# Optimization experiments

Hardware: AMD Instinct MI355X
Metric: run time of the kernel (lower is better)

The kernel has to match this reference:

```python
import jax, jax.numpy as jnp
import numpy as np

N_NODES = 100000
N_EDGES = 1600000
D_IN = 256
D_OUT = 128


def setup_inputs() -> dict:
    key = jax.random.key(0)
    k1, k2, k3, k4, k5, k6 = jax.random.split(key, 6)
    inp = {
        "input": jax.random.normal(k1, (N_NODES, D_IN), dtype=jnp.float32),
        "edge_row": jax.random.randint(k2, (N_EDGES,), 0, N_NODES),
        "edge_col": jax.random.randint(k3, (N_EDGES,), 0, N_NODES),
        "edge_val": jax.random.uniform(k4, (N_EDGES,), dtype=jnp.float32),
        "W": jax.random.normal(k5, (D_IN, D_OUT), dtype=jnp.float32) * (1.0 / np.sqrt(D_IN)),
        "b": jax.random.normal(k6, (D_OUT,), dtype=jnp.float32) * 0.01,
    }
    return inp


def reference(input, edge_row, edge_col, edge_val, W, b):
    # support = Linear(input)  -> [N, D_OUT]
    support = jnp.dot(input, W) + b
    # sparse.mm(adj, support): out[r] = sum_e val[e] * support[col[e]] for edges with row[e]==r
    msgs = edge_val[:, None] * support[edge_col]  # [E, D_OUT]
    agg = jax.ops.segment_sum(msgs, edge_row, num_segments=N_NODES)  # [N, D_OUT]
    return jnp.tanh(agg)
```

## Files before the change

### kernel.cpp

```cpp
#include <hip/hip_runtime.h>
#include <math.h>

#define N_NODES 100000
#define N_EDGES 1600000
#define D_IN 256
#define D_OUT 128

#define OFF_SUPPORT 0
#define OFF_COUNTS  51200000
#define OFF_CSREV   51600008
#define OFF_BSUMS   64400008
#define OFF_WTHI    64400416
#define OFF_WTLO    64465952

#define SCAN_CHUNK  1024
#define SCAN_BLOCKS ((N_NODES + SCAN_CHUNK - 1) / SCAN_CHUNK)

#define GB 128
#define GEMM_BLOCKS ((N_NODES + GB - 1) / GB)
#define EDGE_BLOCKS ((N_EDGES + 255) / 256)
#define WCONV_BLOCKS ((D_IN * D_OUT) / 256)

typedef __attribute__((ext_vector_type(8))) short s8v;
typedef __attribute__((ext_vector_type(4))) float f4v;

__device__ __forceinline__ short f2bf(float x) {
  unsigned u = __float_as_uint(x);
  unsigned r = u + 0x7FFF + ((u >> 16) & 1);
  return (short)(r >> 16);
}
__device__ __forceinline__ float bf2f(short h) {
  return __uint_as_float(((unsigned)(unsigned short)h) << 16);
}

__device__ __forceinline__ void cvt8(float4 a, float4 b, s8v& h, s8v& l) {
  float f[8] = {a.x, a.y, a.z, a.w, b.x, b.y, b.z, b.w};
#pragma unroll
  for (int i = 0; i < 8; i++) {
    short hh = f2bf(f[i]);
    h[i] = hh;
    l[i] = f2bf(f[i] - bf2f(hh));
  }
}

__device__ __forceinline__ void gload_lds16(const void* g, void* l) {
  __builtin_amdgcn_global_load_lds(
      (const __attribute__((address_space(1))) void*)g,
      (__attribute__((address_space(3))) void*)l, 16, 0, 0);
}

#define VMW(N)                                             \
  asm volatile("s_waitcnt vmcnt(" #N ")" ::: "memory");    \
  __builtin_amdgcn_sched_barrier(0)
#define SBAR()                    \
  __builtin_amdgcn_s_barrier();   \
  __builtin_amdgcn_sched_barrier(0)

__global__ __launch_bounds__(256) void prep_kernel(
    const float* __restrict__ W, short* __restrict__ wt_hi,
    short* __restrict__ wt_lo, const int* __restrict__ erow,
    int* __restrict__ counts) {
  if (blockIdx.x < WCONV_BLOCKS) {
    int idx = blockIdx.x * 256 + threadIdx.x;
    int k = idx >> 7;
    int n = idx & 127;
    float v = W[idx];
    short h = f2bf(v);
    wt_hi[n * 256 + k] = h;
    wt_lo[n * 256 + k] = f2bf(v - bf2f(h));
  } else {
    int e = (blockIdx.x - WCONV_BLOCKS) * 256 + threadIdx.x;
    if (e < N_EDGES) atomicAdd(&counts[erow[e]], 1);
  }
}

__global__ __launch_bounds__(256, 2) void gemm_kernel(
    const float* __restrict__ input, const short* __restrict__ wt_hi,
    const short* __restrict__ wt_lo, const float* __restrict__ b,
    float* __restrict__ support) {
  __shared__ short Bh[2][128][64];
  __shared__ short Bl[2][128][64];
  const int t = threadIdx.x;
  const int lane = t & 63;
  const int wv = t >> 6;
  const int qm = lane & 15;
  const int quad = lane >> 4;
  const int node0 = blockIdx.x * GB;

  int r0 = node0 + wv * 32 + qm;
  int r1 = r0 + 16;
  if (r0 > N_NODES - 1) r0 = N_NODES - 1;
  if (r1 > N_NODES - 1) r1 = N_NODES - 1;
  const float* a0p = input + (size_t)r0 * D_IN + quad * 8;
  const float* a1p = input + (size_t)r1 * D_IN + quad * 8;

  const int lrow = lane >> 3;
  const int lpc = lane & 7;
  auto stageB = [&](int q, int p) {
    const int rb = wv * 32;
#pragma unroll
    for (int j = 0; j < 4; ++j) {
      int n = rb + j * 8 + lrow;
      int sc = lpc ^ (n & 7);
      const short* sh = wt_hi + (size_t)n * 256 + q * 64 + sc * 8;
      const short* sl = wt_lo + (size_t)n * 256 + q * 64 + sc * 8;
      gload_lds16(sh, &Bh[p][rb + j * 8][0]);
      gload_lds16(sl, &Bl[p][rb + j * 8][0]);
    }
  };

  float4 A0[4], A1[4], A2[4];
  auto loadA = [&](float4* d, int s) {
    d[0] = *(const float4*)(a0p + s * 32);
    d[1] = *(const float4*)(a0p + s * 32 + 4);
    d[2] = *(const float4*)(a1p + s * 32);
    d[3] = *(const float4*)(a1p + s * 32 + 4);
  };

  f4v acc[2][8];
#pragma unroll
  for (int mt = 0; mt < 2; mt++)
#pragma unroll
    for (int nt = 0; nt < 8; nt++) acc[mt][nt] = (f4v){0.f, 0.f, 0.f, 0.f};

  s8v ah0, al0, ah1, al1;
  auto cvtA = [&](const float4* X) {
    cvt8(X[0], X[1], ah0, al0);
    cvt8(X[2], X[3], ah1, al1);
  };
  auto mfma8 = [&](int p, int si) {
#pragma unroll
    for (int nt = 0; nt < 8; ++nt) {
      int n = nt * 16 + qm;
      int pc = (si * 4 + quad) ^ (n & 7);
      s8v bh = *(const s8v*)&Bh[p][n][pc * 8];
      s8v bl = *(const s8v*)&Bl[p][n][pc * 8];
      acc[0][nt] = __builtin_amdgcn_mfma_f32_16x16x32_bf16(ah0, bh, acc[0][nt], 0, 0, 0);
      acc[0][nt] = __builtin_amdgcn_mfma_f32_16x16x32_bf16(ah0, bl, acc[0][nt], 0, 0, 0);
      acc[0][nt] = __builtin_amdgcn_mfma_f32_16x16x32_bf16(al0, bh, acc[0][nt], 0, 0, 0);
      acc[1][nt] = __builtin_amdgcn_mfma_f32_16x16x32_bf16(ah1, bh, acc[1][nt], 0, 0, 0);
      acc[1][nt] = __builtin_amdgcn_mfma_f32_16x16x32_bf16(ah1, bl, acc[1][nt], 0, 0, 0);
      acc[1][nt] = __builtin_amdgcn_mfma_f32_16x16x32_bf16(al1, bh, acc[1][nt], 0, 0, 0);
    }
  };

  stageB(0, 0);
  loadA(A0, 0);
  loadA(A1, 1);
  loadA(A2, 2);
  VMW(8);
  SBAR();
  cvtA(A0);
  stageB(1, 1);
  loadA(A0, 3);
  mfma8(0, 0);
  VMW(16);
  cvtA(A1);
  loadA(A1, 4);
  mfma8(0, 1);
  VMW(8);
  SBAR();
  cvtA(A2);
  stageB(2, 0);
  loadA(A2, 5);
  mfma8(1, 0);
  VMW(16);
  cvtA(A0);
  loadA(A0, 6);
  mfma8(1, 1);
  VMW(8);
  SBAR();
  cvtA(A1);
  stageB(3, 1);
  loadA(A1, 7);
  mfma8(0, 0);
  VMW(16);
  cvtA(A2);
  mfma8(0, 1);
  VMW(4);
  SBAR();
  cvtA(A0);
  mfma8(1, 0);
  VMW(0);
  cvtA(A1);
  mfma8(1, 1);

  float bias[8];
#pragma unroll
  for (int nt = 0; nt < 8; nt++) bias[nt] = b[nt * 16 + qm];
#pragma unroll
  for (int mt = 0; mt < 2; mt++) {
#pragma unroll
    for (int nt = 0; nt < 8; nt++) {
      int col = nt * 16 + qm;
#pragma unroll
      for (int r = 0; r < 4; r++) {
        int node = node0 + wv * 32 + mt * 16 + quad * 4 + r;
        if (node < N_NODES)
          support[(size_t)node * D_OUT + col] = acc[mt][nt][r] + bias[nt];
      }
    }
  }
}

__global__ __launch_bounds__(256) void build_kernel(
    const int* __restrict__ erow, const int* __restrict__ ecol,
    const float* __restrict__ eval, const int* __restrict__ offsets,
    int* __restrict__ fill, int2* __restrict__ csr_ev) {
  int e = blockIdx.x * 256 + threadIdx.x;
  if (e < N_EDGES) {
    int r = erow[e];
    int idx = offsets[r] + atomicAdd(&fill[r], 1);
    csr_ev[idx] = make_int2(ecol[e], __float_as_int(eval[e]));
  }
}

__global__ __launch_bounds__(256) void scan_phase1(const int* __restrict__ counts,
                                                   int* __restrict__ bsums) {
  __shared__ int ts[256];
  int t = threadIdx.x;
  int idx0 = blockIdx.x * SCAN_CHUNK + t * 4;
  int s = 0;
#pragma unroll
  for (int i = 0; i < 4; i++)
    if (idx0 + i < N_NODES) s += counts[idx0 + i];
  ts[t] = s;
  __syncthreads();
#pragma unroll
  for (int off = 128; off > 0; off >>= 1) {
    if (t < off) ts[t] += ts[t + off];
    __syncthreads();
  }
  if (t == 0) bsums[blockIdx.x] = ts[0];
}

__global__ __launch_bounds__(128) void scan_phase2(int* __restrict__ bsums) {
  __shared__ int s[128];
  int t = threadIdx.x;
  int v = (t < SCAN_BLOCKS) ? bsums[t] : 0;
  s[t] = v;
  __syncthreads();
#pragma unroll
  for (int off = 1; off < 128; off <<= 1) {
    int x = (t >= off) ? s[t - off] : 0;
    __syncthreads();
    s[t] += x;
    __syncthreads();
  }
  if (t < SCAN_BLOCKS) bsums[t] = s[t] - v;
}

__global__ __launch_bounds__(256) void scan_phase3(int* __restrict__ counts,
                                                   const int* __restrict__ bsums,
                                                   int* __restrict__ fill) {
  __shared__ int ts[256];
  int t = threadIdx.x;
  int b = blockIdx.x;
  int idx0 = b * SCAN_CHUNK + t * 4;
  int v[4];
  int s = 0;
#pragma unroll
  for (int i = 0; i < 4; i++) {
    v[i] = (idx0 + i < N_NODES) ? counts[idx0 + i] : 0;
    s += v[i];
  }
  ts[t] = s;
  __syncthreads();
#pragma unroll
  for (int off = 1; off < 256; off <<= 1) {
    int x = (t >= off) ? ts[t - off] : 0;
    __syncthreads();
    ts[t] += x;
    __syncthreads();
  }
  int run = bsums[b] + ts[t] - s;
#pragma unroll
  for (int i = 0; i < 4; i++) {
    int idx = idx0 + i;
    if (idx < N_NODES) {
      counts[idx] = run;
      fill[idx] = 0;
    }
    run += v[i];
  }
  if (b == 0 && t == 0) counts[N_NODES] = N_EDGES;
}

__global__ __launch_bounds__(256) void agg_kernel(
    const int* __restrict__ offsets, const int2* __restrict__ csr_ev,
    const float* __restrict__ support, float* __restrict__ out) {
  int r = blockIdx.x * 8 + (threadIdx.x >> 5);
  int l4 = (threadIdx.x & 31) * 4;
  int beg = offsets[r];
  int end = offsets[r + 1];
  float4 acc = make_float4(0.f, 0.f, 0.f, 0.f);

  if (end > beg) {
    int2 e[8], en[8];
#pragma unroll
    for (int u = 0; u < 8; u++) {
      int idx = beg + u;
      int c = idx < end ? idx : end - 1;
      e[u] = csr_ev[c];
      if (idx >= end) e[u].y = 0;
    }
    for (int j = beg; j < end; j += 8) {
      int jn = j + 8;
      if (jn < end) {
#pragma unroll
        for (int u = 0; u < 8; u++) {
          int idx = jn + u;
          int c = idx < end ? idx : end - 1;
          en[u] = csr_ev[c];
          if (idx >= end) en[u].y = 0;
        }
      }
      float4 s[8];
#pragma unroll
      for (int u = 0; u < 8; u++)
        s[u] = *(const float4*)(support + (size_t)e[u].x * D_OUT + l4);
#pragma unroll
      for (int u = 0; u < 8; u++) {
        float v = __int_as_float(e[u].y);
        acc.x = fmaf(v, s[u].x, acc.x);
        acc.y = fmaf(v, s[u].y, acc.y);
        acc.z = fmaf(v, s[u].z, acc.z);
        acc.w = fmaf(v, s[u].w, acc.w);
      }
#pragma unroll
      for (int u = 0; u < 8; u++) e[u] = en[u];
    }
  }
  *(float4*)(out + (size_t)r * D_OUT + l4) =
      make_float4(tanhf(acc.x), tanhf(acc.y), tanhf(acc.z), tanhf(acc.w));
}

extern "C" void kernel_launch(void* const* d_in, const int* in_sizes, int n_in,
                              void* d_out, int out_size, void* d_ws, size_t ws_size,
                              hipStream_t stream) {
  const float* input = (const float*)d_in[0];
  const int* erow = (const int*)d_in[1];
  const int* ecol = (const int*)d_in[2];
  const float* eval = (const float*)d_in[3];
  const float* W = (const float*)d_in[4];
  const float* b = (const float*)d_in[5];
  float* out = (float*)d_out;

  char* ws = (char*)d_ws;
  float* support = (float*)(ws + OFF_SUPPORT);
  int* counts = (int*)(ws + OFF_COUNTS);
  int2* csr_ev = (int2*)(ws + OFF_CSREV);
  int* bsums = (int*)(ws + OFF_BSUMS);
  short* wt_hi = (short*)(ws + OFF_WTHI);
  short* wt_lo = (short*)(ws + OFF_WTLO);
  int* fill = (int*)d_out;

  hipMemsetAsync(ws + OFF_COUNTS, 0, (size_t)(N_NODES + 1) * 4, stream);

  hipLaunchKernelGGL(prep_kernel, dim3(WCONV_BLOCKS + EDGE_BLOCKS), dim3(256),
                     0, stream, W, wt_hi, wt_lo, erow, counts);
  hipLaunchKernelGGL(gemm_kernel, dim3(GEMM_BLOCKS), dim3(256), 0, stream,
                     input, wt_hi, wt_lo, b, support);
  hipLaunchKernelGGL(scan_phase1, dim3(SCAN_BLOCKS), dim3(256), 0, stream,
                     counts, bsums);
  hipLaunchKernelGGL(scan_phase2, dim3(1), dim3(128), 0, stream, bsums);
  hipLaunchKernelGGL(scan_phase3, dim3(SCAN_BLOCKS), dim3(256), 0, stream,
                     counts, bsums, fill);
  hipLaunchKernelGGL(build_kernel, dim3(EDGE_BLOCKS), dim3(256), 0, stream,
                     erow, ecol, eval, counts, fill, csr_ev);
  hipLaunchKernelGGL(agg_kernel, dim3(N_NODES / 8), dim3(256), 0, stream,
                     counts, csr_ev, support, out);
}
```

Baseline: 464.5 us.

## Fuse edge histogram into GEMM launch and reuse atomic positions in CSR build

The separate memset is removed; the counts array is now zeroed inside the weight-conversion kernel. The row-count histogram moves from the prep launch into the GEMM launch as extra blocks, so the atomics run alongside the matrix multiply. Each edge's atomicAdd return value is saved in a per-edge position array held in the output buffer, which removes the second round of atomics in the build kernel and the fill reset in the scan. Build and agg also switch to nontemporal loads and stores on packed 64-bit edge records. The cost is an extra 6.4MB position array write and read, and GEMM blocks share their launch with atomic-heavy blocks.

```diff
diff --git a/kernel.cpp b/kernel.cpp
--- a/kernel.cpp
+++ b/kernel.cpp
@@ -19,7 +19,6 @@
 #define GB 128
 #define GEMM_BLOCKS ((N_NODES + GB - 1) / GB)
 #define EDGE_BLOCKS ((N_EDGES + 255) / 256)
-#define WCONV_BLOCKS ((D_IN * D_OUT) / 256)
 
 typedef __attribute__((ext_vector_type(8))) short s8v;
 typedef __attribute__((ext_vector_type(4))) float f4v;
@@ -56,26 +55,21 @@
   __builtin_amdgcn_s_barrier();   \
   __builtin_amdgcn_sched_barrier(0)
 
-__global__ __launch_bounds__(256) void prep_kernel(
+__global__ __launch_bounds__(256) void wconv_kernel(
     const float* __restrict__ W, short* __restrict__ wt_hi,
-    short* __restrict__ wt_lo, const int* __restrict__ erow,
-    int* __restrict__ counts) {
-  if (blockIdx.x < WCONV_BLOCKS) {
-    int idx = blockIdx.x * 256 + threadIdx.x;
-    int k = idx >> 7;
-    int n = idx & 127;
-    float v = W[idx];
-    short h = f2bf(v);
-    wt_hi[n * 256 + k] = h;
-    wt_lo[n * 256 + k] = f2bf(v - bf2f(h));
-  } else {
-    int e = (blockIdx.x - WCONV_BLOCKS) * 256 + threadIdx.x;
-    if (e < N_EDGES) atomicAdd(&counts[erow[e]], 1);
-  }
-}
-
-__global__ __launch_bounds__(256, 2) void gemm_kernel(
-    const float* __restrict__ input, const short* __restrict__ wt_hi,
+    short* __restrict__ wt_lo, int* __restrict__ counts) {
+  int idx = blockIdx.x * 256 + threadIdx.x;
+  int k = idx >> 7;
+  int n = idx & 127;
+  float v = W[idx];
+  short h = f2bf(v);
+  wt_hi[n * 256 + k] = h;
+  wt_lo[n * 256 + k] = f2bf(v - bf2f(h));
+  for (int i = idx; i < N_NODES + 1; i += 32768) counts[i] = 0;
+}
+
+__device__ __forceinline__ void gemm_body(
+    int gb, const float* __restrict__ input, const short* __restrict__ wt_hi,
     const short* __restrict__ wt_lo, const float* __restrict__ b,
     float* __restrict__ support) {
   __shared__ short Bh[2][128][64];
@@ -85,7 +79,7 @@
   const int wv = t >> 6;
   const int qm = lane & 15;
   const int quad = lane >> 4;
-  const int node0 = blockIdx.x * GB;
+  const int node0 = gb * GB;
 
   int r0 = node0 + wv * 32 + qm;
   int r1 = r0 + 16;
@@ -203,15 +197,32 @@
   }
 }
 
+__global__ __launch_bounds__(256, 2) void gemm_hist_kernel(
+    const float* __restrict__ input, const short* __restrict__ wt_hi,
+    const short* __restrict__ wt_lo, const float* __restrict__ b,
+    float* __restrict__ support, const int* __restrict__ erow,
+    int* __restrict__ counts, int* __restrict__ pos_e) {
+  if (blockIdx.x < GEMM_BLOCKS) {
+    gemm_body(blockIdx.x, input, wt_hi, wt_lo, b, support);
+  } else {
+    int e = (blockIdx.x - GEMM_BLOCKS) * 256 + threadIdx.x;
+    if (e < N_EDGES) pos_e[e] = atomicAdd(&counts[erow[e]], 1);
+  }
+}
+
 __global__ __launch_bounds__(256) void build_kernel(
     const int* __restrict__ erow, const int* __restrict__ ecol,
     const float* __restrict__ eval, const int* __restrict__ offsets,
-    int* __restrict__ fill, int2* __restrict__ csr_ev) {
+    const int* __restrict__ pos_e, long long* __restrict__ csr_ev) {
   int e = blockIdx.x * 256 + threadIdx.x;
   if (e < N_EDGES) {
-    int r = erow[e];
-    int idx = offsets[r] + atomicAdd(&fill[r], 1);
-    csr_ev[idx] = make_int2(ecol[e], __float_as_int(eval[e]));
+    int r = __builtin_nontemporal_load(erow + e);
+    int c = __builtin_nontemporal_load(ecol + e);
+    int vb = __builtin_nontemporal_load((const int*)eval + e);
+    int p = __builtin_nontemporal_load(pos_e + e);
+    int idx = offsets[r] + p;
+    long long packed = (unsigned int)c | ((long long)(unsigned int)vb << 32);
+    __builtin_nontemporal_store(packed, csr_ev + idx);
   }
 }
 
@@ -251,8 +262,7 @@
 }
 
 __global__ __launch_bounds__(256) void scan_phase3(int* __restrict__ counts,
-                                                   const int* __restrict__ bsums,
-                                                   int* __restrict__ fill) {
+                                                   const int* __restrict__ bsums) {
   __shared__ int ts[256];
   int t = threadIdx.x;
   int b = blockIdx.x;
@@ -277,17 +287,14 @@
 #pragma unroll
   for (int i = 0; i < 4; i++) {
     int idx = idx0 + i;
-    if (idx < N_NODES) {
-      counts[idx] = run;
-      fill[idx] = 0;
-    }
+    if (idx < N_NODES) counts[idx] = run;
     run += v[i];
   }
   if (b == 0 && t == 0) counts[N_NODES] = N_EDGES;
 }
 
 __global__ __launch_bounds__(256) void agg_kernel(
-    const int* __restrict__ offsets, const int2* __restrict__ csr_ev,
+    const int* __restrict__ offsets, const long long* __restrict__ csr_ev,
     const float* __restrict__ support, float* __restrict__ out) {
   int r = blockIdx.x * 8 + (threadIdx.x >> 5);
   int l4 = (threadIdx.x & 31) * 4;
@@ -296,13 +303,15 @@
   float4 acc = make_float4(0.f, 0.f, 0.f, 0.f);
 
   if (end > beg) {
-    int2 e[8], en[8];
+    int ec[8], encol[8];
+    float ev[8], env[8];
 #pragma unroll
     for (int u = 0; u < 8; u++) {
       int idx = beg + u;
       int c = idx < end ? idx : end - 1;
-      e[u] = csr_ev[c];
-      if (idx >= end) e[u].y = 0;
+      long long p = __builtin_nontemporal_load(csr_ev + c);
+      ec[u] = (int)(unsigned int)p;
+      ev[u] = (idx < end) ? __uint_as_float((unsigned int)(p >> 32)) : 0.f;
     }
     for (int j = beg; j < end; j += 8) {
       int jn = j + 8;
@@ -311,24 +320,24 @@
         for (int u = 0; u < 8; u++) {
           int idx = jn + u;
           int c = idx < end ? idx : end - 1;
-          en[u] = csr_ev[c];
-          if (idx >= end) en[u].y = 0;
+          long long p = __builtin_nontemporal_load(csr_ev + c);
+          encol[u] = (int)(unsigned int)p;
+          env[u] = (idx < end) ? __uint_as_float((unsigned int)(p >> 32)) : 0.f;
         }
       }
       float4 s[8];
 #pragma unroll
       for (int u = 0; u < 8; u++)
-        s[u] = *(const float4*)(support + (size_t)e[u].x * D_OUT + l4);
+        s[u] = *(const float4*)(support + (size_t)ec[u] * D_OUT + l4);
 #pragma unroll
       for (int u = 0; u < 8; u++) {
-        float v = __int_as_float(e[u].y);
-        acc.x = fmaf(v, s[u].x, acc.x);
-        acc.y = fmaf(v, s[u].y, acc.y);
-        acc.z = fmaf(v, s[u].z, acc.z);
-        acc.w = fmaf(v, s[u].w, acc.w);
+        acc.x = fmaf(ev[u], s[u].x, acc.x);
+        acc.y = fmaf(ev[u], s[u].y, acc.y);
+        acc.z = fmaf(ev[u], s[u].z, acc.z);
+        acc.w = fmaf(ev[u], s[u].w, acc.w);
       }
 #pragma unroll
-      for (int u = 0; u < 8; u++) e[u] = en[u];
+      for (int u = 0; u < 8; u++) { ec[u] = encol[u]; ev[u] = env[u]; }
     }
   }
   *(float4*)(out + (size_t)r * D_OUT + l4) =
@@ -349,25 +358,24 @@
   char* ws = (char*)d_ws;
   float* support = (float*)(ws + OFF_SUPPORT);
   int* counts = (int*)(ws + OFF_COUNTS);
-  int2* csr_ev = (int2*)(ws + OFF_CSREV);
+  long long* csr_ev = (long long*)(ws + OFF_CSREV);
   int* bsums = (int*)(ws + OFF_BSUMS);
   short* wt_hi = (short*)(ws + OFF_WTHI);
   short* wt_lo = (short*)(ws + OFF_WTLO);
-  int* fill = (int*)d_out;
-
-  hipMemsetAsync(ws + OFF_COUNTS, 0, (size_t)(N_NODES + 1) * 4, stream);
-
-  hipLaunchKernelGGL(prep_kernel, dim3(WCONV_BLOCKS + EDGE_BLOCKS), dim3(256),
-                     0, stream, W, wt_hi, wt_lo, erow, counts);
-  hipLaunchKernelGGL(gemm_kernel, dim3(GEMM_BLOCKS), dim3(256), 0, stream,
-                     input, wt_hi, wt_lo, b, support);
+  int* pos_e = (int*)d_out;
+
+  hipLaunchKernelGGL(wconv_kernel, dim3((D_IN * D_OUT) / 256), dim3(256), 0,
+                     stream, W, wt_hi, wt_lo, counts);
+  hipLaunchKernelGGL(gemm_hist_kernel, dim3(GEMM_BLOCKS + EDGE_BLOCKS),
+                     dim3(256), 0, stream, input, wt_hi, wt_lo, b, support,
+                     erow, counts, pos_e);
   hipLaunchKernelGGL(scan_phase1, dim3(SCAN_BLOCKS), dim3(256), 0, stream,
                      counts, bsums);
   hipLaunchKernelGGL(scan_phase2, dim3(1), dim3(128), 0, stream, bsums);
   hipLaunchKernelGGL(scan_phase3, dim3(SCAN_BLOCKS), dim3(256), 0, stream,
-                     counts, bsums, fill);
+                     counts, bsums);
   hipLaunchKernelGGL(build_kernel, dim3(EDGE_BLOCKS), dim3(256), 0, stream,
-                     erow, ecol, eval, counts, fill, csr_ev);
+                     erow, ecol, eval, counts, pos_e, csr_ev);
   hipLaunchKernelGGL(agg_kernel, dim3(N_NODES / 8), dim3(256), 0, stream,
                      counts, csr_ev, support, out);
 }
```

After: 422.4 us. 9.1% less time.
